# Optimization experiments

Measured on AMD Instinct MI355X. Metric: run time of the kernel, lower is better.

Reference implementation:

```python
import jax, jax.numpy as jnp
import numpy as np

B = 16384            # rays per chunk
NUM_BINS = 129       # num_samples + 1 fenceposts
RESAMPLE_PADDING = 0.01


def setup_inputs() -> dict:
    key = jax.random.key(0)
    k1, k2, k3, k4, k5 = jax.random.split(key, 5)
    origins = jax.random.normal(k1, (B, 3), dtype=jnp.float32)
    d = jax.random.normal(k2, (B, 3), dtype=jnp.float32)
    directions = d / jnp.linalg.norm(d, axis=-1, keepdims=True)
    radii = jax.random.uniform(k3, (B, 1), dtype=jnp.float32, minval=0.001, maxval=0.005)
    # sorted fencepost distances in [near=2, far=6]
    t_vals = jnp.sort(jax.random.uniform(k4, (B, NUM_BINS), dtype=jnp.float32, minval=2.0, maxval=6.0), axis=-1)
    weights = jax.random.uniform(k5, (B, NUM_BINS - 1), dtype=jnp.float32)
    return dict(origins=origins, directions=directions, radii=radii, t_vals=t_vals, weights=weights)


def _piecewise_constant_pdf(bins, weights, num_samples):
    """Inverse-CDF sampling (randomized=False). Math identical to the torch
    mask/max/min formulation: searchsorted(cdf, u, 'right') gives the first
    index with cdf > u (the min over ~mask), and idx-1 the last index with
    cdf <= u (the max over mask); u in [0, 1-eps) so indices are in range."""
    eps = 1e-5
    wsum = jnp.sum(weights, axis=-1, keepdims=True)
    pad = jnp.maximum(0.0, eps - wsum)
    weights = weights + pad / weights.shape[-1]
    wsum = wsum + pad
    pdf = weights / wsum
    cdf = jnp.minimum(1.0, jnp.cumsum(pdf[..., :-1], axis=-1))
    cdf = jnp.concatenate([jnp.zeros_like(cdf[..., :1]), cdf, jnp.ones_like(cdf[..., :1])], axis=-1)  # [B, bins]
    u = jnp.linspace(0.0, 1.0 - jnp.finfo(jnp.float32).eps, num_samples, dtype=jnp.float32)
    u = jnp.broadcast_to(u, cdf.shape[:-1] + (num_samples,))
    idx1 = jax.vmap(lambda c, uu: jnp.searchsorted(c, uu, side='right'))(cdf, u)
    idx1 = jnp.clip(idx1, 1, cdf.shape[-1] - 1)
    idx0 = idx1 - 1
    take = lambda x, i: jnp.take_along_axis(x, i, axis=-1)
    bins_g0, bins_g1 = take(bins, idx0), take(bins, idx1)
    cdf_g0, cdf_g1 = take(cdf, idx0), take(cdf, idx1)
    t = jnp.clip(jnp.nan_to_num((u - cdf_g0) / (cdf_g1 - cdf_g0), nan=0.0), 0.0, 1.0)
    return bins_g0 + t * (bins_g1 - bins_g0)


def _conical_frustum_to_gaussian(d, t0, t1, base_radius):
    """Stable cone->Gaussian (diag covariance), lifted along ray axis d."""
    mu = (t0 + t1) / 2
    hw = (t1 - t0) / 2
    denom = 3 * mu ** 2 + hw ** 2
    t_mean = mu + 2 * mu * hw ** 2 / denom
    t_var = hw ** 2 / 3 - 4 / 15 * (hw ** 4 * (12 * mu ** 2 - hw ** 2) / denom ** 2)
    r_var = base_radius ** 2 * (mu ** 2 / 4 + 5 / 12 * hw ** 2 - 4 / 15 * hw ** 4 / denom)
    mean = d[..., None, :] * t_mean[..., None]                       # [B, S, 3]
    d_mag_sq = jnp.sum(d ** 2, axis=-1, keepdims=True) + 1e-10
    d_outer_diag = d ** 2
    null_outer_diag = 1 - d_outer_diag / d_mag_sq
    cov_diag = t_var[..., None] * d_outer_diag[..., None, :] + r_var[..., None] * null_outer_diag[..., None, :]
    return mean, cov_diag


def reference(origins, directions, radii, t_vals, weights):
    # blur weights (max-pool then avg of neighbors) + padding
    wpad = jnp.concatenate([weights[..., :1], weights, weights[..., -1:]], axis=-1)
    wmax = jnp.maximum(wpad[..., :-1], wpad[..., 1:])
    wblur = 0.5 * (wmax[..., :-1] + wmax[..., 1:])
    w = wblur + RESAMPLE_PADDING
    # stop_grad=True in the torch module (torch.no_grad around resampling)
    new_t_vals = jax.lax.stop_gradient(_piecewise_constant_pdf(t_vals, w, t_vals.shape[-1]))
    t0, t1 = new_t_vals[..., :-1], new_t_vals[..., 1:]
    means, covs = _conical_frustum_to_gaussian(directions, t0, t1, radii)
    means = means + origins[..., None, :]
    return new_t_vals, means, covs
```

## Files before the change

kernel.cpp:

```cpp
#include <hip/hip_runtime.h>

#define NRAYS 16384
#define NB 129
#define NW 128

__global__ __launch_bounds__(256) void mipnerf_block_kernel(
    const float* __restrict__ origins,
    const float* __restrict__ directions,
    const float* __restrict__ radii,
    const float* __restrict__ t_vals,
    const float* __restrict__ weights,
    float* __restrict__ out_t,
    float* __restrict__ out_means,
    float* __restrict__ out_covs)
{
    __shared__ __align__(16) float s_t  [4 * NB];
    __shared__ __align__(16) float s_w  [4 * NW];
    __shared__ __align__(16) float s_cdf[4 * NB];
    __shared__ __align__(16) float s_nt [4 * NB];
    __shared__ __align__(16) float s_mean[4 * NW * 3];
    __shared__ __align__(16) float s_cov [4 * NW * 3];

    const int tid = threadIdx.x;
    const int wv  = tid >> 6;
    const int l   = tid & 63;
    const int blk = blockIdx.x;
    const int ray = (blk << 2) + wv;

    if (tid < NB)
        reinterpret_cast<float4*>(s_t)[tid] =
            reinterpret_cast<const float4*>(t_vals + (long)blk * (4 * NB))[tid];
    if (tid < NW)
        reinterpret_cast<float4*>(s_w)[tid] =
            reinterpret_cast<const float4*>(weights + (long)blk * (4 * NW))[tid];
    __syncthreads();

    const float* wrow = s_w + wv * NW;
    const float w0  = wrow[2 * l];
    const float w1  = wrow[2 * l + 1];
    const float wm1 = (l == 0)  ? w0 : wrow[2 * l - 1];
    const float wp1 = (l == 63) ? w1 : wrow[2 * l + 2];

    const float mx01 = fmaxf(w0, w1);
    const float wb0 = 0.5f * (fmaxf(wm1, w0) + mx01) + 0.01f;
    const float wb1 = 0.5f * (mx01 + fmaxf(w1, wp1)) + 0.01f;

    float S = wb0 + wb1;
    #pragma unroll
    for (int off = 1; off < 64; off <<= 1) {
        const float t = __shfl_up(S, off);
        if (l >= off) S += t;
    }
    const float W1 = S;
    const float W0 = S - wb1;
    const float inv_wsum = 1.0f / __shfl(S, 63);

    float* cdf = s_cdf + wv * NB;
    cdf[2 * l + 1] = fminf(1.0f, W0 * inv_wsum);
    if (l < 63) cdf[2 * l + 2] = fminf(1.0f, W1 * inv_wsum);
    if (l == 0)  cdf[0]      = 0.0f;
    if (l == 63) cdf[NB - 1] = 1.0f;
    __builtin_amdgcn_wave_barrier();

    const float* bins = s_t + wv * NB;
    const float ueps = 1.0f - 1.1920929e-7f;
    const float step = ueps / 128.0f;

    auto sampleAt = [&](float u) -> float {
        int lo = 0, hi = NB;
        while (lo < hi) {
            const int mid = (lo + hi) >> 1;
            if (cdf[mid] <= u) lo = mid + 1; else hi = mid;
        }
        const int i1 = lo;
        const int i0 = i1 - 1;
        const float c0 = cdf[i0], c1 = cdf[i1];
        const float b0 = bins[i0], b1 = bins[i1];
        float tt = (u - c0) / (c1 - c0);
        if (tt != tt) tt = 0.0f;
        tt = fminf(fmaxf(tt, 0.0f), 1.0f);
        return fmaf(tt, b1 - b0, b0);
    };

    float* ntrow = s_nt + wv * NB;
    ntrow[l]      = sampleAt((float)l * step);
    ntrow[64 + l] = sampleAt((float)(64 + l) * step);
    if (l == 63) ntrow[128] = sampleAt(ueps);
    __builtin_amdgcn_wave_barrier();

    const float n0 = ntrow[2 * l];
    const float n1 = ntrow[2 * l + 1];
    const float n2 = ntrow[2 * l + 2];

    const float dx = directions[ray * 3 + 0];
    const float dy = directions[ray * 3 + 1];
    const float dz = directions[ray * 3 + 2];
    const float ox = origins[ray * 3 + 0];
    const float oy = origins[ray * 3 + 1];
    const float oz = origins[ray * 3 + 2];
    const float rad = radii[ray];
    const float rad2 = rad * rad;
    const float dx2 = dx * dx, dy2 = dy * dy, dz2 = dz * dz;
    const float inv_dms = 1.0f / (dx2 + dy2 + dz2 + 1e-10f);
    const float nxо = 1.0f - dx2 * inv_dms;
    const float nyо = 1.0f - dy2 * inv_dms;
    const float nzо = 1.0f - dz2 * inv_dms;

    float* mrow = s_mean + wv * (NW * 3) + 6 * l;
    float* crow = s_cov  + wv * (NW * 3) + 6 * l;
    const float tt0[2] = { n0, n1 };
    const float tt1[2] = { n1, n2 };
    #pragma unroll
    for (int k = 0; k < 2; ++k) {
        const float mu = 0.5f * (tt0[k] + tt1[k]);
        const float hw = 0.5f * (tt1[k] - tt0[k]);
        const float mu2 = mu * mu, hw2 = hw * hw;
        const float inv_denom = 1.0f / (3.0f * mu2 + hw2);
        const float t_mean = mu + 2.0f * mu * hw2 * inv_denom;
        const float t_var  = hw2 * (1.0f / 3.0f)
                           - (4.0f / 15.0f) * (hw2 * hw2 * (12.0f * mu2 - hw2) * inv_denom * inv_denom);
        const float r_var  = rad2 * (0.25f * mu2 + (5.0f / 12.0f) * hw2
                                     - (4.0f / 15.0f) * hw2 * hw2 * inv_denom);
        mrow[3 * k + 0] = fmaf(dx, t_mean, ox);
        mrow[3 * k + 1] = fmaf(dy, t_mean, oy);
        mrow[3 * k + 2] = fmaf(dz, t_mean, oz);
        crow[3 * k + 0] = fmaf(t_var, dx2, r_var * nxо);
        crow[3 * k + 1] = fmaf(t_var, dy2, r_var * nyо);
        crow[3 * k + 2] = fmaf(t_var, dz2, r_var * nzо);
    }
    __syncthreads();

    if (tid < NB)
        reinterpret_cast<float4*>(out_t + (long)blk * (4 * NB))[tid] =
            reinterpret_cast<const float4*>(s_nt)[tid];

    float4* om4 = reinterpret_cast<float4*>(out_means + (long)blk * (4 * NW * 3));
    float4* oc4 = reinterpret_cast<float4*>(out_covs  + (long)blk * (4 * NW * 3));
    const float4* sm4 = reinterpret_cast<const float4*>(s_mean);
    const float4* sc4 = reinterpret_cast<const float4*>(s_cov);
    #pragma unroll
    for (int i = tid; i < 4 * NW * 3 / 4; i += 256) {
        om4[i] = sm4[i];
        oc4[i] = sc4[i];
    }
}

extern "C" void kernel_launch(void* const* d_in, const int* in_sizes, int n_in,
                              void* d_out, int out_size, void* d_ws, size_t ws_size,
                              hipStream_t stream) {
    const float* origins    = (const float*)d_in[0];
    const float* directions = (const float*)d_in[1];
    const float* radii      = (const float*)d_in[2];
    const float* t_vals     = (const float*)d_in[3];
    const float* weights    = (const float*)d_in[4];

    float* out_t     = (float*)d_out;
    float* out_means = out_t + (long)NRAYS * NB;
    float* out_covs  = out_means + (long)NRAYS * NW * 3;

    const int grid = NRAYS / 4;
    mipnerf_block_kernel<<<grid, 256, 0, stream>>>(
        origins, directions, radii, t_vals, weights, out_t, out_means, out_covs);
}
```

Measured before the change: 22.54 us.

## Replace per-sample CDF binary search with per-interval inverse scatter of samples

Instead of each lane binary-searching a shared-memory CDF for every uniform sample, each lane keeps its own CDF interval endpoints in registers. It works out which sample indices fall in each interval with ceil(c/step) and writes the interpolated samples directly into the shared sample row. This drops the CDF shared buffer and the logarithmic chain of dependent LDS reads. In exchange, loop trip counts vary per lane, which causes divergence, and the float rounding at interval boundaries may differ slightly from searchsorted semantics.

```diff
diff --git a/kernel.cpp b/kernel.cpp
--- a/kernel.cpp
+++ b/kernel.cpp
@@ -4,7 +4,7 @@
 #define NB 129
 #define NW 128
 
-__global__ __launch_bounds__(256) void mipnerf_block_kernel(
+__global__ __launch_bounds__(256) void mipnerf_inv_kernel(
     const float* __restrict__ origins,
     const float* __restrict__ directions,
     const float* __restrict__ radii,
@@ -16,7 +16,6 @@
 {
     __shared__ __align__(16) float s_t  [4 * NB];
     __shared__ __align__(16) float s_w  [4 * NW];
-    __shared__ __align__(16) float s_cdf[4 * NB];
     __shared__ __align__(16) float s_nt [4 * NB];
     __shared__ __align__(16) float s_mean[4 * NW * 3];
     __shared__ __align__(16) float s_cov [4 * NW * 3];
@@ -55,37 +54,41 @@
     const float W0 = S - wb1;
     const float inv_wsum = 1.0f / __shfl(S, 63);
 
-    float* cdf = s_cdf + wv * NB;
-    cdf[2 * l + 1] = fminf(1.0f, W0 * inv_wsum);
-    if (l < 63) cdf[2 * l + 2] = fminf(1.0f, W1 * inv_wsum);
-    if (l == 0)  cdf[0]      = 0.0f;
-    if (l == 63) cdf[NB - 1] = 1.0f;
-    __builtin_amdgcn_wave_barrier();
+    const float c_lo  = (l == 0)  ? 0.0f : fminf(1.0f, (W0 - wb0) * inv_wsum);
+    const float c_mid = fminf(1.0f, W0 * inv_wsum);
+    const float c_hi  = (l == 63) ? 1.0f : fminf(1.0f, W1 * inv_wsum);
 
     const float* bins = s_t + wv * NB;
-    const float ueps = 1.0f - 1.1920929e-7f;
-    const float step = ueps / 128.0f;
+    const float b0 = bins[2 * l];
+    const float b1 = bins[2 * l + 1];
+    const float b2 = bins[2 * l + 2];
 
-    auto sampleAt = [&](float u) -> float {
-        int lo = 0, hi = NB;
-        while (lo < hi) {
-            const int mid = (lo + hi) >> 1;
-            if (cdf[mid] <= u) lo = mid + 1; else hi = mid;
-        }
-        const int i1 = lo;
-        const int i0 = i1 - 1;
-        const float c0 = cdf[i0], c1 = cdf[i1];
-        const float b0 = bins[i0], b1 = bins[i1];
-        float tt = (u - c0) / (c1 - c0);
-        if (tt != tt) tt = 0.0f;
-        tt = fminf(fmaxf(tt, 0.0f), 1.0f);
-        return fmaf(tt, b1 - b0, b0);
-    };
+    const float ueps     = 1.0f - 1.1920929e-7f;
+    const float step     = ueps / 128.0f;
+    const float inv_step = 128.0f / ueps;
+    const int s0 = (int)ceilf(c_lo  * inv_step);
+    const int s1 = (int)ceilf(c_mid * inv_step);
+    const int s2 = (int)ceilf(c_hi  * inv_step);
 
     float* ntrow = s_nt + wv * NB;
-    ntrow[l]      = sampleAt((float)l * step);
-    ntrow[64 + l] = sampleAt((float)(64 + l) * step);
-    if (l == 63) ntrow[128] = sampleAt(ueps);
+    {
+        const float inv_d = 1.0f / (c_mid - c_lo);
+        const float db = b1 - b0;
+        for (int s = s0; s < s1; ++s) {
+            float tt = ((float)s * step - c_lo) * inv_d;
+            tt = fminf(fmaxf(tt, 0.0f), 1.0f);
+            ntrow[s] = fmaf(tt, db, b0);
+        }
+    }
+    {
+        const float inv_d = 1.0f / (c_hi - c_mid);
+        const float db = b2 - b1;
+        for (int s = s1; s < s2; ++s) {
+            float tt = ((float)s * step - c_mid) * inv_d;
+            tt = fminf(fmaxf(tt, 0.0f), 1.0f);
+            ntrow[s] = fmaf(tt, db, b1);
+        }
+    }
     __builtin_amdgcn_wave_barrier();
 
     const float n0 = ntrow[2 * l];
@@ -102,9 +105,9 @@
     const float rad2 = rad * rad;
     const float dx2 = dx * dx, dy2 = dy * dy, dz2 = dz * dz;
     const float inv_dms = 1.0f / (dx2 + dy2 + dz2 + 1e-10f);
-    const float nxо = 1.0f - dx2 * inv_dms;
-    const float nyо = 1.0f - dy2 * inv_dms;
-    const float nzо = 1.0f - dz2 * inv_dms;
+    const float nullx = 1.0f - dx2 * inv_dms;
+    const float nully = 1.0f - dy2 * inv_dms;
+    const float nullz = 1.0f - dz2 * inv_dms;
 
     float* mrow = s_mean + wv * (NW * 3) + 6 * l;
     float* crow = s_cov  + wv * (NW * 3) + 6 * l;
@@ -124,9 +127,9 @@
         mrow[3 * k + 0] = fmaf(dx, t_mean, ox);
         mrow[3 * k + 1] = fmaf(dy, t_mean, oy);
         mrow[3 * k + 2] = fmaf(dz, t_mean, oz);
-        crow[3 * k + 0] = fmaf(t_var, dx2, r_var * nxо);
-        crow[3 * k + 1] = fmaf(t_var, dy2, r_var * nyо);
-        crow[3 * k + 2] = fmaf(t_var, dz2, r_var * nzо);
+        crow[3 * k + 0] = fmaf(t_var, dx2, r_var * nullx);
+        crow[3 * k + 1] = fmaf(t_var, dy2, r_var * nully);
+        crow[3 * k + 2] = fmaf(t_var, dz2, r_var * nullz);
     }
     __syncthreads();
 
@@ -159,6 +162,6 @@
     float* out_covs  = out_means + (long)NRAYS * NW * 3;
 
     const int grid = NRAYS / 4;
-    mipnerf_block_kernel<<<grid, 256, 0, stream>>>(
+    mipnerf_inv_kernel<<<grid, 256, 0, stream>>>(
         origins, directions, radii, t_vals, weights, out_t, out_means, out_covs);
 }
```

Result: faster. 19.56 us (-13.2%).
